# Optimization experiments

Measured on AMD Instinct MI355X. Metric: run time of the kernel, lower is better.

Reference implementation:

```python
import jax, jax.numpy as jnp
import numpy as np

B, N, E, H = 8, 1500, 3000, 256
HOPS = 3


def setup_inputs() -> dict:
    key = jax.random.key(0)
    ks = jax.random.split(key, 9)
    node_state = jax.random.normal(ks[0], (B, N, H), jnp.float32)
    edge_vec = jax.random.normal(ks[1], (B, E, H), jnp.float32)
    # sparse-ish 0/1 incidence matrices (avg ~3 nonzeros per row)
    node2edge = (jax.random.uniform(ks[2], (B, E, N)) < 0.002).astype(jnp.float32)
    edge2node = (jax.random.uniform(ks[3], (B, N, E)) < 0.002).astype(jnp.float32)
    s = 1.0 / np.sqrt(H).astype(np.float32)
    W_max = jax.random.uniform(ks[4], (H, H), jnp.float32, -s, s)        # linear_max, no bias
    W_fz = jax.random.uniform(ks[5], (4 * H, H), jnp.float32, -s, s)     # gated fusion
    b_fz = jnp.zeros((H,), jnp.float32)
    W_z = jax.random.uniform(ks[6], (2 * H, H), jnp.float32, -s, s)      # GRU gates, no bias
    W_r = jax.random.uniform(ks[7], (2 * H, H), jnp.float32, -s, s)
    W_t = jax.random.uniform(ks[8], (2 * H, H), jnp.float32, -s, s)
    return dict(node_state=node_state, edge_vec=edge_vec, node2edge=node2edge,
                edge2node=edge2node, W_max=W_max, W_fz=W_fz, b_fz=b_fz,
                W_z=W_z, W_r=W_r, W_t=W_t)


def _msg_pass(node_state, edge_vec, n2e, e2n):
    # n2e: (B,E,N), e2n: (B,N,E)
    edge_emb = jnp.einsum('ben,bnh->beh', n2e, node_state) + edge_vec   # (B,E,H)
    norm = jnp.sum(e2n, axis=2, keepdims=True) + 1.0                     # self-loop degree norm
    return (jnp.einsum('bne,beh->bnh', e2n, edge_emb) + node_state) / norm


def _gated_fusion(h, x, W_fz, b_fz):
    z = jax.nn.sigmoid(jnp.concatenate([h, x, h * x, h - x], -1) @ W_fz + b_fz)
    return (1.0 - z) * h + z * x


def _gru_step(h, x, W_z, W_r, W_t):
    hx = jnp.concatenate([h, x], -1)
    z = jax.nn.sigmoid(hx @ W_z)
    r = jax.nn.sigmoid(hx @ W_r)
    t = jnp.tanh(jnp.concatenate([r * h, x], -1) @ W_t)
    return (1.0 - z) * h + z * t


def reference(node_state, edge_vec, node2edge, edge2node, W_max, W_fz, b_fz, W_z, W_r, W_t):
    n2e_T = jnp.swapaxes(node2edge, 1, 2)   # (B,N,E)
    e2n_T = jnp.swapaxes(edge2node, 1, 2)   # (B,E,N)
    for _ in range(HOPS):
        bw = _msg_pass(node_state, edge_vec, node2edge, edge2node)
        fw = _msg_pass(node_state, edge_vec, e2n_T, n2e_T)
        agg = _gated_fusion(fw, bw, W_fz, b_fz)
        node_state = _gru_step(node_state, agg, W_z, W_r, W_t)
    # graph max pool: linear then max over nodes
    graph_embedding = jnp.max(node_state @ W_max, axis=1)[None]  # (1,B,H)
    return jnp.swapaxes(node_state, 0, 1), graph_embedding       # (N,B,H), (1,B,H)
```

## Files before the change

### kernel.cpp

```cpp
#include <hip/hip_runtime.h>
#include <hip/hip_bf16.h>
#include <stdint.h>

#define Bb 8
#define Nn 1500
#define Ee 3000
#define Hh 256
#define NHOPS 3
#define CAP 32
#define Mrows (Bb*Nn)
#define BE (Bb*Ee)
#define BN (Bb*Nn)
#define TOTQ 9000000

typedef __bf16 bf16x8 __attribute__((ext_vector_type(8)));
typedef float f32x4 __attribute__((ext_vector_type(4)));
typedef float nf4 __attribute__((ext_vector_type(4)));

__device__ __forceinline__ float sigmoidf_(float x){ return 1.f/(1.f+__expf(-x)); }

__device__ __forceinline__ unsigned short f2b(float f){
  union { float f; unsigned int u; } x; x.f = f;
  unsigned int r = (x.u + 0x7fffu + ((x.u >> 16) & 1u)) >> 16;
  return (unsigned short)r;
}
__device__ __forceinline__ float b2f(unsigned short u){
  union { unsigned int u; float f; } x; x.u = ((unsigned int)u) << 16;
  return x.f;
}
__device__ __forceinline__ ushort4 pack4(float4 v){
  return make_ushort4(f2b(v.x), f2b(v.y), f2b(v.z), f2b(v.w));
}
__device__ __forceinline__ float4 unpack4(ushort4 u){
  return make_float4(b2f(u.x), b2f(u.y), b2f(u.z), b2f(u.w));
}
__device__ __forceinline__ unsigned fkey(float f){
  unsigned u = __float_as_uint(f);
  return (u & 0x80000000u) ? ~u : (u | 0x80000000u);
}

#define GLL16(g, l) __builtin_amdgcn_global_load_lds( \
    (const __attribute__((address_space(1))) unsigned int*)(g), \
    (__attribute__((address_space(3))) unsigned int*)(l), 16, 0, 0)

__device__ __forceinline__ void scan_proc(nf4 vv, int t,
    int* __restrict__ Aidx, int* __restrict__ cntA, int* __restrict__ Didx, int* __restrict__ cntD,
    int* __restrict__ Bidx, int* __restrict__ cntB, int* __restrict__ Cidx, int* __restrict__ cntC) {
  if (vv.x == 0.f && vv.y == 0.f && vv.z == 0.f && vv.w == 0.f) return;
  int *rowIdx, *rowCnt, *colIdx, *colCnt;
  int g, q, R, C;
  if (t < TOTQ) {
    rowIdx = Aidx; rowCnt = cntA; colIdx = Didx; colCnt = cntD;
    R = Ee; C = Nn;
    g = t / 375; q = t - g * 375;
  } else {
    int tt = t - TOTQ;
    rowIdx = Bidx; rowCnt = cntB; colIdx = Cidx; colCnt = cntC;
    R = Nn; C = Ee;
    g = tt / 750; q = tt - g * 750;
  }
  int b = g / R;
  int r = g - b * R;
  int cbase = q * 4;
  #pragma unroll
  for (int j = 0; j < 4; ++j) {
    float vj = (j == 0) ? vv.x : (j == 1) ? vv.y : (j == 2) ? vv.z : vv.w;
    if (vj != 0.f) {
      int c = cbase + j;
      int rs = atomicAdd(&rowCnt[g], 1);
      if (rs < CAP) rowIdx[(size_t)g * CAP + rs] = c;
      int cs = atomicAdd(&colCnt[b * C + c], 1);
      if (cs < CAP) colIdx[(size_t)(b * C + c) * CAP + cs] = r;
    }
  }
}

__global__ void preprocess_kernel(const nf4* __restrict__ n2e4, const nf4* __restrict__ e2n4,
                                  int* __restrict__ Aidx, int* __restrict__ cntA,
                                  int* __restrict__ Didx, int* __restrict__ cntD,
                                  int* __restrict__ Bidx, int* __restrict__ cntB,
                                  int* __restrict__ Cidx, int* __restrict__ cntC,
                                  const float* __restrict__ Wfz, const float* __restrict__ Wz,
                                  const float* __restrict__ Wr, const float* __restrict__ Wt,
                                  const float* __restrict__ Wmax,
                                  unsigned short* __restrict__ WfzT, unsigned short* __restrict__ WzrT,
                                  unsigned short* __restrict__ WtT, unsigned short* __restrict__ WmaxT,
                                  const float* __restrict__ in_ns, unsigned short* __restrict__ nsb,
                                  const float* __restrict__ in_ev, unsigned short* __restrict__ evb) {
  int bx = blockIdx.x;
  if (bx < 8790) {
    int t0 = bx * 2048 + threadIdx.x;
    nf4 v[8];
    int ts[8];
    #pragma unroll
    for (int r2 = 0; r2 < 8; ++r2) {
      int t = t0 + r2 * 256;
      ts[r2] = t;
      const nf4* p = (t < TOTQ) ? (n2e4 + t) : (e2n4 + (t - TOTQ));
      if (t < 2 * TOTQ) v[r2] = __builtin_nontemporal_load(p);
      else { v[r2].x = 0.f; v[r2].y = 0.f; v[r2].z = 0.f; v[r2].w = 0.f; }
    }
    __builtin_amdgcn_sched_barrier(0);
    #pragma unroll
    for (int r2 = 0; r2 < 8; ++r2)
      scan_proc(v[r2], ts[r2], Aidx, cntA, Didx, cntD, Bidx, cntB, Cidx, cntC);
  } else if (bx < 11350) {
    int t = (bx - 8790) * 256 + threadIdx.x;
    if (t < 196608) {
      int n = t / 768, k = t % 768;
      float v;
      if (k < 256)      v = Wfz[k * 256 + n] + Wfz[(k + 768) * 256 + n];
      else if (k < 512) v = Wfz[k * 256 + n] - Wfz[(k + 512) * 256 + n];
      else              v = Wfz[k * 256 + n];
      WfzT[t] = f2b(v);
    } else if (t < 458752) {
      int u = t - 196608;
      int j = u >> 9, k = u & 511;
      float v = (j < 256) ? Wz[k * 256 + j] : Wr[k * 256 + (j - 256)];
      WzrT[u] = f2b(v);
    } else if (t < 589824) {
      int u = t - 458752;
      int n = u >> 9, k = u & 511;
      WtT[u] = f2b(Wt[k * 256 + n]);
    } else if (t < 655360) {
      int u = t - 589824;
      int n = u >> 8, k = u & 255;
      WmaxT[u] = f2b(Wmax[k * 256 + n]);
    }
  } else if (bx < 12100) {
    int t0 = (bx - 11350) * 1024 + threadIdx.x;
    #pragma unroll
    for (int r = 0; r < 4; ++r) {
      int t = t0 + r * 256;
      ((ushort4*)nsb)[t] = pack4(((const float4*)in_ns)[t]);
    }
  } else {
    int t0 = (bx - 12100) * 1024 + threadIdx.x;
    #pragma unroll
    for (int r = 0; r < 4; ++r) {
      int t = t0 + r * 256;
      ((ushort4*)evb)[t] = pack4(((const float4*)in_ev)[t]);
    }
  }
}

__device__ __forceinline__ void sort_one(int* pp, int c) {
  if (c > CAP) c = CAP;
  int v[CAP];
  for (int j = 0; j < c; ++j) v[j] = pp[j];
  for (int j = 1; j < c; ++j) { int key = v[j]; int k = j - 1;
    while (k >= 0 && v[k] > key) { v[k+1] = v[k]; --k; } v[k+1] = key; }
  for (int j = 0; j < c; ++j) pp[j] = v[j];
}
__global__ void sort4_kernel(int* __restrict__ Cidx, const int* __restrict__ cntC,
                             int* __restrict__ Didx, const int* __restrict__ cntD,
                             int* __restrict__ Aidx, const int* __restrict__ cntA,
                             int* __restrict__ Bidx, const int* __restrict__ cntB) {
  int i = blockIdx.x * 256 + threadIdx.x;
  if (i < BE) sort_one(Cidx + (size_t)i * CAP, cntC[i]);
  else if (i < BE + BN) { int k = i - BE; sort_one(Didx + (size_t)k * CAP, cntD[k]); }
  else if (i < 2 * BE + BN) { int k = i - BE - BN; sort_one(Aidx + (size_t)k * CAP, cntA[k]); }
  else if (i < 2 * BE + 2 * BN) { int k = i - 2 * BE - BN; sort_one(Bidx + (size_t)k * CAP, cntB[k]); }
}

__global__ void edge_kernel(const ushort4* __restrict__ evb4, const ushort4* __restrict__ nsb4,
                            const int* __restrict__ Aidx, const int* __restrict__ Acnt,
                            const int* __restrict__ Cidx, const int* __restrict__ Ccnt,
                            ushort4* __restrict__ eb4, ushort4* __restrict__ ef4) {
  int w = __builtin_amdgcn_readfirstlane((int)(threadIdx.x >> 6));
  int be = blockIdx.x * 4 + w;
  int lane = threadIdx.x & 63;
  int b = be / Ee;
  int cA = min(Acnt[be], CAP), cC = min(Ccnt[be], CAP);
  const int* pA = Aidx + (size_t)be * CAP;
  const int* pC = Cidx + (size_t)be * CAP;
  float4 ev = unpack4(evb4[(size_t)be * 64 + lane]);
  float4 sA = ev, sC = ev;
  for (int i = 0; i < cA; ++i) {
    int n = pA[i];
    float4 t = unpack4(nsb4[((size_t)b * Nn + n) * 64 + lane]);
    sA.x += t.x; sA.y += t.y; sA.z += t.z; sA.w += t.w;
  }
  for (int i = 0; i < cC; ++i) {
    int n = pC[i];
    float4 t = unpack4(nsb4[((size_t)b * Nn + n) * 64 + lane]);
    sC.x += t.x; sC.y += t.y; sC.z += t.z; sC.w += t.w;
  }
  eb4[(size_t)be * 64 + lane] = pack4(sA);
  ef4[(size_t)be * 64 + lane] = pack4(sC);
}

__global__ void node_kernel(const ushort4* __restrict__ nsb4,
                            const ushort4* __restrict__ eb4, const ushort4* __restrict__ ef4,
                            const int* __restrict__ Bidx, const int* __restrict__ Bcnt,
                            const int* __restrict__ Didx, const int* __restrict__ Dcnt,
                            ushort4* __restrict__ Xfz4) {
  int w = __builtin_amdgcn_readfirstlane((int)(threadIdx.x >> 6));
  int bn = blockIdx.x * 4 + w;
  int lane = threadIdx.x & 63;
  int b = bn / Nn;
  int rB = Bcnt[bn], rD = Dcnt[bn];
  int cB = min(rB, CAP), cD = min(rD, CAP);
  const int* pB = Bidx + (size_t)bn * CAP;
  const int* pD = Didx + (size_t)bn * CAP;
  float4 h0 = unpack4(nsb4[(size_t)bn * 64 + lane]);
  float4 sb = h0, sf = h0;
  for (int i = 0; i < cB; ++i) {
    int e = pB[i];
    float4 t = unpack4(eb4[((size_t)b * Ee + e) * 64 + lane]);
    sb.x += t.x; sb.y += t.y; sb.z += t.z; sb.w += t.w;
  }
  for (int i = 0; i < cD; ++i) {
    int e = pD[i];
    float4 t = unpack4(ef4[((size_t)b * Ee + e) * 64 + lane]);
    sf.x += t.x; sf.y += t.y; sf.z += t.z; sf.w += t.w;
  }
  float ib = 1.f / (1.f + (float)rB), idf = 1.f / (1.f + (float)rD);
  sb.x *= ib; sb.y *= ib; sb.z *= ib; sb.w *= ib;
  sf.x *= idf; sf.y *= idf; sf.z *= idf; sf.w *= idf;
  float4 prod = make_float4(sf.x*sb.x, sf.y*sb.y, sf.z*sb.z, sf.w*sb.w);
  size_t m = bn;
  Xfz4[m * 192 +   0 + lane] = pack4(sf);
  Xfz4[m * 192 +  64 + lane] = pack4(sb);
  Xfz4[m * 192 + 128 + lane] = pack4(prod);
}

#define EPI_MAXR 0
#define EPI_FZ   1
#define EPI_ZR   2
#define EPI_GRU  3

template<int EPI, int LAST, int SPLIT, int NBLK>
__global__ __launch_bounds__(256) void gemm_kernel(
    const unsigned short* __restrict__ A0, const unsigned short* __restrict__ A1,
    const unsigned short* __restrict__ WT,
    int M, int K,
    unsigned* __restrict__ gkey, const float* __restrict__ bfz,
    unsigned short* __restrict__ aggb, unsigned short* __restrict__ zbuf,
    unsigned short* __restrict__ rhb,
    float* __restrict__ outNBH,
    unsigned short* __restrict__ nsbout)
{
  __shared__ unsigned short As[64 * 64];
  __shared__ unsigned short Bs[64 * 64];
  __shared__ unsigned redk[2][64];
  int id = blockIdx.x;
  int kgrp = id >> 3;
  int n0 = (kgrp & (NBLK - 1)) * 64;
  int mb = (id & 7) + 8 * (kgrp / NBLK);
  int m0 = mb * 64;
  if (m0 >= M) return;
  int tid = threadIdx.x;
  int lane = tid & 63;
  int wid = __builtin_amdgcn_readfirstlane(tid >> 6);
  int wm = wid >> 1, wn = wid & 1;
  int p = lane >> 4;
  int q = lane & 7;
  int lr = lane >> 3;
  if (EPI == EPI_MAXR && tid < 128) redk[tid >> 6][tid & 63] = 0u;
  f32x4 acc[2][2] = {};
  for (int k0 = 0; k0 < K; k0 += 64) {
    const unsigned short* srcA = A0;
    int kA = k0, sA = K;
    if (SPLIT) { sA = 256; if (k0 >= 256) { srcA = A1; kA = k0 - 256; } }
    {
      int rl0 = wid * 16 + lr;
      int gm0 = m0 + rl0; if (gm0 > M - 1) gm0 = M - 1;
      GLL16(srcA + (size_t)gm0 * sA + kA + ((q ^ (rl0 & 7)) << 3), &As[(wid * 16) * 64]);
      int rl1 = rl0 + 8;
      int gm1 = m0 + rl1; if (gm1 > M - 1) gm1 = M - 1;
      GLL16(srcA + (size_t)gm1 * sA + kA + ((q ^ (rl1 & 7)) << 3), &As[(wid * 16 + 8) * 64]);
      GLL16(WT + (size_t)(n0 + rl0) * K + k0 + ((q ^ (rl0 & 7)) << 3), &Bs[(wid * 16) * 64]);
      GLL16(WT + (size_t)(n0 + rl1) * K + k0 + ((q ^ (rl1 & 7)) << 3), &Bs[(wid * 16 + 8) * 64]);
    }
    __syncthreads();
    #pragma unroll
    for (int kk = 0; kk < 64; kk += 32) {
      int cq = (kk >> 3) + p;
      int ra0 = wm * 32 + (lane & 15);
      int ra1 = ra0 + 16;
      int rb0 = wn * 32 + (lane & 15);
      int rb1 = rb0 + 16;
      bf16x8 a0 = *(const bf16x8*)&As[ra0 * 64 + ((cq ^ (ra0 & 7)) << 3)];
      bf16x8 a1 = *(const bf16x8*)&As[ra1 * 64 + ((cq ^ (ra1 & 7)) << 3)];
      bf16x8 b0 = *(const bf16x8*)&Bs[rb0 * 64 + ((cq ^ (rb0 & 7)) << 3)];
      bf16x8 b1 = *(const bf16x8*)&Bs[rb1 * 64 + ((cq ^ (rb1 & 7)) << 3)];
      acc[0][0] = __builtin_amdgcn_mfma_f32_16x16x32_bf16(a0, b0, acc[0][0], 0, 0, 0);
      acc[0][1] = __builtin_amdgcn_mfma_f32_16x16x32_bf16(a0, b1, acc[0][1], 0, 0, 0);
      acc[1][0] = __builtin_amdgcn_mfma_f32_16x16x32_bf16(a1, b0, acc[1][0], 0, 0, 0);
      acc[1][1] = __builtin_amdgcn_mfma_f32_16x16x32_bf16(a1, b1, acc[1][1], 0, 0, 0);
    }
    __syncthreads();
  }
  if (EPI == EPI_MAXR) {
    int blo = m0 / Nn;
    int bnd = (blo + 1) * Nn;
    #pragma unroll
    for (int ni = 0; ni < 2; ++ni) {
      unsigned um0 = 0u, um1 = 0u;
      #pragma unroll
      for (int mi = 0; mi < 2; ++mi)
      #pragma unroll
      for (int j = 0; j < 4; ++j) {
        int m = m0 + wm * 32 + mi * 16 + p * 4 + j;
        if (m < M) {
          unsigned k = fkey(acc[mi][ni][j]);
          if (m >= bnd) um1 = max(um1, k); else um0 = max(um0, k);
        }
      }
      int cl = wn * 32 + ni * 16 + (lane & 15);
      if (um0) atomicMax(&redk[0][cl], um0);
      if (um1) atomicMax(&redk[1][cl], um1);
    }
    __syncthreads();
    if (tid < 128) {
      int g = tid >> 6, cl = tid & 63;
      unsigned k = redk[g][cl];
      if (k) {
        int mm = (g == 0) ? m0 : (m0 + 63 < M ? m0 + 63 : M - 1);
        atomicMax(&gkey[(mm / Nn) * 256 + n0 + cl], k);
      }
    }
    return;
  }
  #pragma unroll
  for (int mi = 0; mi < 2; ++mi)
  #pragma unroll
  for (int ni = 0; ni < 2; ++ni)
  #pragma unroll
  for (int j = 0; j < 4; ++j) {
    int m = m0 + wm * 32 + mi * 16 + p * 4 + j;
    int c = n0 + wn * 32 + ni * 16 + (lane & 15);
    if (m >= M) continue;
    float v = acc[mi][ni][j];
    if (EPI == EPI_FZ) {
      float z = sigmoidf_(v + bfz[c]);
      float fw = b2f(A0[(size_t)m * K + c]);
      float bw = b2f(A0[(size_t)m * K + 256 + c]);
      aggb[(size_t)m * 256 + c] = f2b((1.f - z) * fw + z * bw);
    } else if (EPI == EPI_ZR) {
      float s = sigmoidf_(v);
      if (c < 256) {
        zbuf[(size_t)m * 256 + c] = f2b(s);
      } else {
        int cz = c - 256;
        rhb[(size_t)m * 256 + cz] = f2b(s * b2f(nsbout[(size_t)m * 256 + cz]));
      }
    } else {
      float t = tanhf(v);
      float zz = b2f(zbuf[(size_t)m * 256 + c]);
      float h = b2f(nsbout[(size_t)m * 256 + c]);
      float nh = (1.f - zz) * h + zz * t;
      nsbout[(size_t)m * 256 + c] = f2b(nh);
      if (LAST) {
        int bb = m / Nn, n = m - bb * Nn;
        outNBH[((size_t)n * Bb + bb) * 256 + c] = nh;
      }
    }
  }
}

__global__ void maxfin_kernel(const unsigned* __restrict__ gkey, float* __restrict__ out) {
  int t = blockIdx.x * 256 + threadIdx.x;
  if (t >= Bb * Hh) return;
  unsigned k = gkey[t];
  unsigned u = (k & 0x80000000u) ? (k & 0x7fffffffu) : ~k;
  out[(size_t)Nn * Bb * Hh + t] = __uint_as_float(u);
}

extern "C" void kernel_launch(void* const* d_in, const int* in_sizes, int n_in,
                              void* d_out, int out_size, void* d_ws, size_t ws_size,
                              hipStream_t stream) {
  const float* in_ns   = (const float*)d_in[0];
  const float* in_ev   = (const float*)d_in[1];
  const float* in_n2e  = (const float*)d_in[2];
  const float* in_e2n  = (const float*)d_in[3];
  const float* in_wmax = (const float*)d_in[4];
  const float* in_wfz  = (const float*)d_in[5];
  const float* in_bfz  = (const float*)d_in[6];
  const float* in_wz   = (const float*)d_in[7];
  const float* in_wr   = (const float*)d_in[8];
  const float* in_wt   = (const float*)d_in[9];
  float* out = (float*)d_out;

  char* base = (char*)d_ws;
  size_t off = 0;
  auto alloc = [&](size_t bytes) -> void* {
    void* r = base + off;
    off = (off + bytes + 255) & ~(size_t)255;
    return r;
  };
  int* cnts = (int*)alloc((size_t)(2 * BE + 2 * BN) * 4);
  unsigned* gkey = (unsigned*)alloc(Bb * Hh * 4);
  int* cntC = cnts;
  int* cntD = cnts + BE;
  int* cntA = cnts + BE + BN;
  int* cntB = cnts + BE + BN + BE;
  int* Aidx = (int*)alloc((size_t)BE * CAP * 4);
  int* Bidx = (int*)alloc((size_t)BN * CAP * 4);
  int* Cidx = (int*)alloc((size_t)BE * CAP * 4);
  int* Didx = (int*)alloc((size_t)BN * CAP * 4);
  unsigned short* nsb = (unsigned short*)alloc((size_t)Mrows * Hh * 2);
  unsigned short* evb = (unsigned short*)alloc((size_t)BE * Hh * 2);
  unsigned short* eb = (unsigned short*)alloc((size_t)BE * Hh * 2);
  unsigned short* ef = (unsigned short*)alloc((size_t)BE * Hh * 2);
  unsigned short* Xfz = (unsigned short*)alloc((size_t)Mrows * 768 * 2);
  unsigned short* aggb = (unsigned short*)alloc((size_t)Mrows * 256 * 2);
  unsigned short* rhb  = (unsigned short*)alloc((size_t)Mrows * 256 * 2);
  unsigned short* zbuf = (unsigned short*)alloc((size_t)Mrows * 256 * 2);
  unsigned short* WfzT  = (unsigned short*)alloc(256 * 768 * 2);
  unsigned short* WzrT  = (unsigned short*)alloc(512 * 512 * 2);
  unsigned short* WtT   = (unsigned short*)alloc(256 * 512 * 2);
  unsigned short* WmaxT = (unsigned short*)alloc(256 * 256 * 2);
  (void)ws_size; (void)in_sizes; (void)n_in; (void)out_size;

  hipMemsetAsync(cnts, 0, (size_t)(2 * BE + 2 * BN) * 4 + (size_t)Bb * Hh * 4, stream);

  preprocess_kernel<<<13600, 256, 0, stream>>>(
      (const nf4*)in_n2e, (const nf4*)in_e2n,
      Aidx, cntA, Didx, cntD, Bidx, cntB, Cidx, cntC,
      in_wfz, in_wz, in_wr, in_wt, in_wmax,
      WfzT, WzrT, WtT, WmaxT,
      in_ns, nsb, in_ev, evb);
  sort4_kernel<<<(2 * BE + 2 * BN + 255) / 256, 256, 0, stream>>>(
      Cidx, cntC, Didx, cntD, Aidx, cntA, Bidx, cntB);

  const int g4 = 192 * 4, g8 = 192 * 8;
  for (int hop = 0; hop < NHOPS; ++hop) {
    edge_kernel<<<BE / 4, 256, 0, stream>>>((const ushort4*)evb, (const ushort4*)nsb,
        Aidx, cntA, Cidx, cntC, (ushort4*)eb, (ushort4*)ef);
    node_kernel<<<BN / 4, 256, 0, stream>>>((const ushort4*)nsb,
        (const ushort4*)eb, (const ushort4*)ef,
        Bidx, cntB, Didx, cntD, (ushort4*)Xfz);
    gemm_kernel<EPI_FZ, 0, 0, 4><<<g4, 256, 0, stream>>>(Xfz, nullptr, WfzT, Mrows, 768,
        nullptr, in_bfz, aggb, nullptr, nullptr, nullptr, nullptr);
    gemm_kernel<EPI_ZR, 0, 1, 8><<<g8, 256, 0, stream>>>(nsb, aggb, WzrT, Mrows, 512,
        nullptr, nullptr, nullptr, zbuf, rhb, nullptr, nsb);
    if (hop < NHOPS - 1) {
      gemm_kernel<EPI_GRU, 0, 1, 4><<<g4, 256, 0, stream>>>(rhb, aggb, WtT, Mrows, 512,
          nullptr, nullptr, nullptr, zbuf, nullptr, nullptr, nsb);
    } else {
      gemm_kernel<EPI_GRU, 1, 1, 4><<<g4, 256, 0, stream>>>(rhb, aggb, WtT, Mrows, 512,
          nullptr, nullptr, nullptr, zbuf, nullptr, out, nsb);
    }
  }

  gemm_kernel<EPI_MAXR, 0, 0, 4><<<g4, 256, 0, stream>>>(nsb, nullptr, WmaxT, Mrows, 256,
      gkey, nullptr, nullptr, nullptr, nullptr, nullptr, nullptr);
  maxfin_kernel<<<(Bb * Hh + 255) / 256, 256, 0, stream>>>(gkey, out);
}
```

Baseline: 359.2 us.

## Compact nonzero incidence entries into a pair list before scattering to CSR

The dense incidence scan no longer does global atomics and scattered index writes inline. Each block collects its nonzero flat indices in shared memory, reserves space with one global atomic, and appends them to a compact pair buffer. A separate kernel then decodes each pair and does the row/column count atomics and index writes. This keeps the bandwidth-bound scan free of long-latency scattered atomics. The cost is an extra kernel launch and a bounded pair buffer that silently drops entries if more than 512 nonzeros fall in one block or the total exceeds the buffer size.

After: 428.6 us. 19.3% more time.

```diff
diff --git a/kernel.cpp b/kernel.cpp
--- a/kernel.cpp
+++ b/kernel.cpp
@@ -12,6 +12,8 @@
 #define BE (Bb*Ee)
 #define BN (Bb*Nn)
 #define TOTQ 9000000
+#define NELEM1 36000000
+#define PAIRBUF (1<<20)
 
 typedef __bf16 bf16x8 __attribute__((ext_vector_type(8)));
 typedef float f32x4 __attribute__((ext_vector_type(4)));
@@ -43,43 +45,8 @@
     (const __attribute__((address_space(1))) unsigned int*)(g), \
     (__attribute__((address_space(3))) unsigned int*)(l), 16, 0, 0)
 
-__device__ __forceinline__ void scan_proc(nf4 vv, int t,
-    int* __restrict__ Aidx, int* __restrict__ cntA, int* __restrict__ Didx, int* __restrict__ cntD,
-    int* __restrict__ Bidx, int* __restrict__ cntB, int* __restrict__ Cidx, int* __restrict__ cntC) {
-  if (vv.x == 0.f && vv.y == 0.f && vv.z == 0.f && vv.w == 0.f) return;
-  int *rowIdx, *rowCnt, *colIdx, *colCnt;
-  int g, q, R, C;
-  if (t < TOTQ) {
-    rowIdx = Aidx; rowCnt = cntA; colIdx = Didx; colCnt = cntD;
-    R = Ee; C = Nn;
-    g = t / 375; q = t - g * 375;
-  } else {
-    int tt = t - TOTQ;
-    rowIdx = Bidx; rowCnt = cntB; colIdx = Cidx; colCnt = cntC;
-    R = Nn; C = Ee;
-    g = tt / 750; q = tt - g * 750;
-  }
-  int b = g / R;
-  int r = g - b * R;
-  int cbase = q * 4;
-  #pragma unroll
-  for (int j = 0; j < 4; ++j) {
-    float vj = (j == 0) ? vv.x : (j == 1) ? vv.y : (j == 2) ? vv.z : vv.w;
-    if (vj != 0.f) {
-      int c = cbase + j;
-      int rs = atomicAdd(&rowCnt[g], 1);
-      if (rs < CAP) rowIdx[(size_t)g * CAP + rs] = c;
-      int cs = atomicAdd(&colCnt[b * C + c], 1);
-      if (cs < CAP) colIdx[(size_t)(b * C + c) * CAP + cs] = r;
-    }
-  }
-}
-
 __global__ void preprocess_kernel(const nf4* __restrict__ n2e4, const nf4* __restrict__ e2n4,
-                                  int* __restrict__ Aidx, int* __restrict__ cntA,
-                                  int* __restrict__ Didx, int* __restrict__ cntD,
-                                  int* __restrict__ Bidx, int* __restrict__ cntB,
-                                  int* __restrict__ Cidx, int* __restrict__ cntC,
+                                  int* __restrict__ gpairs, int* __restrict__ gpaircnt,
                                   const float* __restrict__ Wfz, const float* __restrict__ Wz,
                                   const float* __restrict__ Wr, const float* __restrict__ Wt,
                                   const float* __restrict__ Wmax,
@@ -87,23 +54,45 @@
                                   unsigned short* __restrict__ WtT, unsigned short* __restrict__ WmaxT,
                                   const float* __restrict__ in_ns, unsigned short* __restrict__ nsb,
                                   const float* __restrict__ in_ev, unsigned short* __restrict__ evb) {
+  __shared__ int lcnt, lbase;
+  __shared__ int lpairs[512];
   int bx = blockIdx.x;
   if (bx < 8790) {
+    if (threadIdx.x == 0) lcnt = 0;
+    __syncthreads();
     int t0 = bx * 2048 + threadIdx.x;
     nf4 v[8];
-    int ts[8];
     #pragma unroll
     for (int r2 = 0; r2 < 8; ++r2) {
       int t = t0 + r2 * 256;
-      ts[r2] = t;
       const nf4* p = (t < TOTQ) ? (n2e4 + t) : (e2n4 + (t - TOTQ));
       if (t < 2 * TOTQ) v[r2] = __builtin_nontemporal_load(p);
       else { v[r2].x = 0.f; v[r2].y = 0.f; v[r2].z = 0.f; v[r2].w = 0.f; }
     }
     __builtin_amdgcn_sched_barrier(0);
     #pragma unroll
-    for (int r2 = 0; r2 < 8; ++r2)
-      scan_proc(v[r2], ts[r2], Aidx, cntA, Didx, cntD, Bidx, cntB, Cidx, cntC);
+    for (int r2 = 0; r2 < 8; ++r2) {
+      nf4 vv = v[r2];
+      if (vv.x != 0.f || vv.y != 0.f || vv.z != 0.f || vv.w != 0.f) {
+        int t = t0 + r2 * 256;
+        #pragma unroll
+        for (int j = 0; j < 4; ++j) {
+          float vj = (j == 0) ? vv.x : (j == 1) ? vv.y : (j == 2) ? vv.z : vv.w;
+          if (vj != 0.f) {
+            int p = atomicAdd(&lcnt, 1);
+            if (p < 512) lpairs[p] = t * 4 + j;
+          }
+        }
+      }
+    }
+    __syncthreads();
+    int n = min(lcnt, 512);
+    if (threadIdx.x == 0) lbase = (n > 0) ? atomicAdd(gpaircnt, n) : 0;
+    __syncthreads();
+    for (int i = threadIdx.x; i < n; i += 256) {
+      int dst = lbase + i;
+      if (dst < PAIRBUF) gpairs[dst] = lpairs[i];
+    }
   } else if (bx < 11350) {
     int t = (bx - 8790) * 256 + threadIdx.x;
     if (t < 196608) {
@@ -140,6 +129,37 @@
     for (int r = 0; r < 4; ++r) {
       int t = t0 + r * 256;
       ((ushort4*)evb)[t] = pack4(((const float4*)in_ev)[t]);
+    }
+  }
+}
+
+__global__ void pairscatter_kernel(const int* __restrict__ gpairs, const int* __restrict__ gpaircnt,
+                                   int* __restrict__ Aidx, int* __restrict__ cntA,
+                                   int* __restrict__ Didx, int* __restrict__ cntD,
+                                   int* __restrict__ Bidx, int* __restrict__ cntB,
+                                   int* __restrict__ Cidx, int* __restrict__ cntC) {
+  int n = min(*gpaircnt, PAIRBUF);
+  for (int i = blockIdx.x * 256 + threadIdx.x; i < n; i += 1024 * 256) {
+    int e = gpairs[i];
+    if (e < NELEM1) {
+      int g = e / Nn;
+      int c = e - g * Nn;
+      int b = g / Ee;
+      int r = g - b * Ee;
+      int rs = atomicAdd(&cntA[g], 1);
+      if (rs < CAP) Aidx[(size_t)g * CAP + rs] = c;
+      int cs = atomicAdd(&cntD[b * Nn + c], 1);
+      if (cs < CAP) Didx[(size_t)(b * Nn + c) * CAP + cs] = r;
+    } else {
+      int u = e - NELEM1;
+      int g = u / Ee;
+      int c = u - g * Ee;
+      int b = g / Nn;
+      int r = g - b * Nn;
+      int rs = atomicAdd(&cntB[g], 1);
+      if (rs < CAP) Bidx[(size_t)g * CAP + rs] = c;
+      int cs = atomicAdd(&cntC[b * Ee + c], 1);
+      if (cs < CAP) Cidx[(size_t)(b * Ee + c) * CAP + cs] = r;
     }
   }
 }
@@ -392,10 +412,12 @@
   };
   int* cnts = (int*)alloc((size_t)(2 * BE + 2 * BN) * 4);
   unsigned* gkey = (unsigned*)alloc(Bb * Hh * 4);
+  int* gpaircnt = (int*)alloc(256);
   int* cntC = cnts;
   int* cntD = cnts + BE;
   int* cntA = cnts + BE + BN;
   int* cntB = cnts + BE + BN + BE;
+  int* gpairs = (int*)alloc((size_t)PAIRBUF * 4);
   int* Aidx = (int*)alloc((size_t)BE * CAP * 4);
   int* Bidx = (int*)alloc((size_t)BN * CAP * 4);
   int* Cidx = (int*)alloc((size_t)BE * CAP * 4);
@@ -414,14 +436,18 @@
   unsigned short* WmaxT = (unsigned short*)alloc(256 * 256 * 2);
   (void)ws_size; (void)in_sizes; (void)n_in; (void)out_size;
 
-  hipMemsetAsync(cnts, 0, (size_t)(2 * BE + 2 * BN) * 4 + (size_t)Bb * Hh * 4, stream);
+  hipMemsetAsync(cnts, 0,
+                 (size_t)(2 * BE + 2 * BN) * 4 + (size_t)Bb * Hh * 4 + 256, stream);
 
   preprocess_kernel<<<13600, 256, 0, stream>>>(
       (const nf4*)in_n2e, (const nf4*)in_e2n,
-      Aidx, cntA, Didx, cntD, Bidx, cntB, Cidx, cntC,
+      gpairs, gpaircnt,
       in_wfz, in_wz, in_wr, in_wt, in_wmax,
       WfzT, WzrT, WtT, WmaxT,
       in_ns, nsb, in_ev, evb);
+  pairscatter_kernel<<<1024, 256, 0, stream>>>(
+      gpairs, gpaircnt,
+      Aidx, cntA, Didx, cntD, Bidx, cntB, Cidx, cntC);
   sort4_kernel<<<(2 * BE + 2 * BN + 255) / 256, 256, 0, stream>>>(
       Cidx, cntC, Didx, cntD, Aidx, cntA, Bidx, cntB);
 
```
